# Kernel optimization log

Measured on AMD Instinct MI355X. Metric: run time of the kernel, lower is better.

Reference implementation:

```python
import jax, jax.numpy as jnp
import numpy as np

B, C, W, H = 4, 256, 64, 64
K = C // 8      # key_channels = in_channels // 8
O = C           # out_channels = in_channels


def setup_inputs() -> dict:
    key = jax.random.key(0)
    ks = jax.random.split(key, 8)
    x = jax.random.normal(ks[0], (B, C, W, H), dtype=jnp.float32)
    # 1x1 conv weights stored as [out, in]; conv-style fan-in init scale
    s = 1.0 / np.sqrt(C)
    Wq = jax.random.uniform(ks[1], (K, C), minval=-s, maxval=s, dtype=jnp.float32)
    bq = jax.random.uniform(ks[2], (K,), minval=-s, maxval=s, dtype=jnp.float32)
    Wk = jax.random.uniform(ks[3], (K, C), minval=-s, maxval=s, dtype=jnp.float32)
    bk = jax.random.uniform(ks[4], (K,), minval=-s, maxval=s, dtype=jnp.float32)
    Wv = jax.random.uniform(ks[5], (O, C), minval=-s, maxval=s, dtype=jnp.float32)
    bv = jax.random.uniform(ks[6], (O,), minval=-s, maxval=s, dtype=jnp.float32)
    # gamma is zero-init in the module; use a small nonzero value so the
    # attention branch contributes measurably (kernel-testing baseline)
    gamma = 0.1 * jax.random.normal(ks[7], (1,), dtype=jnp.float32)
    return {"x": x, "Wq": Wq, "bq": bq, "Wk": Wk, "bk": bk,
            "Wv": Wv, "bv": bv, "gamma": gamma}


def reference(x, Wq, bq, Wk, bk, Wv, bv, gamma):
    b, c, w, h = x.shape
    n = w * h
    xr = x.reshape(b, c, n)                                   # B,C,N
    # 1x1 convs == per-pixel linear projections
    q = jnp.einsum('kc,bcn->bnk', Wq, xr) + bq                # B,N,K (permuted query)
    k = jnp.einsum('kc,bcn->bkn', Wk, xr) + bk[:, None]       # B,K,N
    energy = jnp.einsum('bnk,bkm->bnm', q, k)                 # B,N,N
    attention = jax.nn.softmax(energy, axis=-1)
    v = jnp.einsum('oc,bcn->bon', Wv, xr) + bv[:, None]       # B,O,N
    # out = bmm(V, attention^T): out[b,o,m] = sum_n V[b,o,n] * attn[b,m,n]
    out = jnp.einsum('bon,bmn->bom', v, attention)
    out = out.reshape(b, O, w, h)
    out = gamma * out + x                                     # true skip connection
    return out, attention
```

## Files before the change

### kernel.cpp

```cpp
#include <hip/hip_runtime.h>

#define NB  4
#define CCH 256
#define NN  4096
#define KD  32
#define OD  256

typedef __attribute__((ext_vector_type(8))) __bf16 bf16x8;
typedef __attribute__((ext_vector_type(4))) float  floatx4;

__device__ __forceinline__ unsigned short f2bf(float f) {
    union { float f; unsigned u; } v; v.f = f;
    unsigned r = v.u + 0x7FFFu + ((v.u >> 16) & 1u);
    return (unsigned short)(r >> 16);
}
__device__ __forceinline__ float bf2f(unsigned short h) {
    union { unsigned u; float f; } v; v.u = ((unsigned)h) << 16;
    return v.f;
}
__device__ __forceinline__ bf16x8 ldfrag(const unsigned short* p) {
    union { bf16x8 v; unsigned u[4]; } r;
    r.u[0] = *(const unsigned*)(p + 0);
    r.u[1] = *(const unsigned*)(p + 2);
    r.u[2] = *(const unsigned*)(p + 4);
    r.u[3] = *(const unsigned*)(p + 6);
    return r.v;
}

#define WPAD 66
#define VPAD 136

__global__ __launch_bounds__(256) void proj_kernel(
    const float* __restrict__ x,
    const float* __restrict__ Wq, const float* __restrict__ bq,
    const float* __restrict__ Wk, const float* __restrict__ bk,
    const float* __restrict__ Wv, const float* __restrict__ bv,
    unsigned short* __restrict__ Qb, unsigned short* __restrict__ Ktb,
    unsigned short* __restrict__ Vb)
{
    __shared__ __align__(16) unsigned char smem[50944];
    unsigned short* Wh   = (unsigned short*)smem;
    unsigned short* Wl   = (unsigned short*)(smem + 8448);
    unsigned short* Xth  = (unsigned short*)(smem + 16896);
    unsigned short* Xtl  = (unsigned short*)(smem + 33792);
    float*          bias = (float*)(smem + 50688);
    unsigned short* Yt = (unsigned short*)(smem + 16896);
    unsigned short* Vt = (unsigned short*)(smem + 16896);

    const int bid = blockIdx.x;
    const int mc  = bid >> 7;
    const int pnl = bid & 127;
    const int nb  = pnl & 31;
    const int b   = pnl >> 5;

    const int tid = threadIdx.x;
    const int wave = tid >> 6;
    const int lane = tid & 63;
    const int quad = lane >> 4;
    const int li   = lane & 15;
    const int pxw  = wave * 32;
    const int px0  = nb * 128;

    const float* xb = x + (size_t)b * CCH * NN;

    floatx4 acc[4][2];
    #pragma unroll
    for (int mf = 0; mf < 4; ++mf)
        #pragma unroll
        for (int nf = 0; nf < 2; ++nf)
            acc[mf][nf] = (floatx4){0.f, 0.f, 0.f, 0.f};

    for (int ks = 0; ks < 4; ++ks) {
        const int c0 = ks * 64;
        __syncthreads();

        #pragma unroll
        for (int i = 0; i < 4; ++i) {
            int idx4 = i * 256 + tid;
            int row  = idx4 >> 4;
            int c4   = (idx4 & 15) * 4;
            const float* src;
            if (mc == 0) src = (row < 32) ? (Wq + row * CCH) : (Wk + (row - 32) * CCH);
            else         src = Wv + ((size_t)((mc - 1) * 64 + row)) * CCH;
            floatx4 w = *(const floatx4*)(src + c0 + c4);
            #pragma unroll
            for (int j = 0; j < 4; ++j) {
                unsigned short h = f2bf(w[j]);
                unsigned short l = f2bf(w[j] - bf2f(h));
                Wh[row * WPAD + c4 + j] = h;
                Wl[row * WPAD + c4 + j] = l;
            }
        }
        #pragma unroll
        for (int i = 0; i < 8; ++i) {
            int idx4 = i * 256 + tid;
            int c    = idx4 >> 5;
            int px   = (idx4 & 31) * 4;
            floatx4 v = *(const floatx4*)(xb + (size_t)(c0 + c) * NN + px0 + px);
            #pragma unroll
            for (int j = 0; j < 4; ++j) {
                unsigned short h = f2bf(v[j]);
                unsigned short l = f2bf(v[j] - bf2f(h));
                Xth[(px + j) * WPAD + c] = h;
                Xtl[(px + j) * WPAD + c] = l;
            }
        }
        if (ks == 0 && tid < 64) {
            float bb;
            if (mc == 0) bb = (tid < 32) ? bq[tid] : bk[tid - 32];
            else         bb = bv[(mc - 1) * 64 + tid];
            bias[tid] = bb;
        }
        __syncthreads();

        #pragma unroll
        for (int kk = 0; kk < 2; ++kk) {
            bf16x8 ah[4], al[4], bh[2], bl[2];
            #pragma unroll
            for (int mf = 0; mf < 4; ++mf) {
                const int ro = (mf * 16 + li) * WPAD + kk * 32 + quad * 8;
                ah[mf] = ldfrag(Wh + ro);
                al[mf] = ldfrag(Wl + ro);
            }
            #pragma unroll
            for (int nf = 0; nf < 2; ++nf) {
                const int ro = (pxw + nf * 16 + li) * WPAD + kk * 32 + quad * 8;
                bh[nf] = ldfrag(Xth + ro);
                bl[nf] = ldfrag(Xtl + ro);
            }
            #pragma unroll
            for (int mf = 0; mf < 4; ++mf)
                #pragma unroll
                for (int nf = 0; nf < 2; ++nf) {
                    acc[mf][nf] = __builtin_amdgcn_mfma_f32_16x16x32_bf16(ah[mf], bh[nf], acc[mf][nf], 0, 0, 0);
                    acc[mf][nf] = __builtin_amdgcn_mfma_f32_16x16x32_bf16(ah[mf], bl[nf], acc[mf][nf], 0, 0, 0);
                    acc[mf][nf] = __builtin_amdgcn_mfma_f32_16x16x32_bf16(al[mf], bh[nf], acc[mf][nf], 0, 0, 0);
                }
        }
    }

    __syncthreads();
    if (mc == 0) {
        #pragma unroll
        for (int mf = 0; mf < 4; ++mf)
            #pragma unroll
            for (int nf = 0; nf < 2; ++nf)
                #pragma unroll
                for (int r = 0; r < 4; ++r) {
                    const int o = mf * 16 + quad * 4 + r;
                    float f = acc[mf][nf][r] + bias[o];
                    Yt[(pxw + nf * 16 + li) * WPAD + o] = f2bf(f);
                }
        __syncthreads();
        if (tid < 128) {
            const int px = tid;
            const size_t n = (size_t)(b * NN + px0 + px);
            unsigned short* qdst = Qb  + n * KD;
            unsigned short* kdst = Ktb + n * KD;
            const unsigned short* src = Yt + px * WPAD;
            #pragma unroll
            for (int i = 0; i < 4; ++i) {
                union { uint4 u4; unsigned u[4]; } q, k;
                #pragma unroll
                for (int j = 0; j < 4; ++j) {
                    q.u[j] = *(const unsigned*)(src + i * 8 + j * 2);
                    k.u[j] = *(const unsigned*)(src + 32 + i * 8 + j * 2);
                }
                *(uint4*)(qdst + i * 8) = q.u4;
                *(uint4*)(kdst + i * 8) = k.u4;
            }
        }
    } else {
        #pragma unroll
        for (int mf = 0; mf < 4; ++mf)
            #pragma unroll
            for (int nf = 0; nf < 2; ++nf)
                #pragma unroll
                for (int r = 0; r < 4; ++r) {
                    const int o = mf * 16 + quad * 4 + r;
                    float f = acc[mf][nf][r] + bias[o];
                    Vt[o * VPAD + pxw + nf * 16 + li] = f2bf(f);
                }
        __syncthreads();
        const int ol   = tid >> 2;
        const int part = tid & 3;
        const unsigned short* src = Vt + ol * VPAD + part * 32;
        unsigned short* dst = Vb + (size_t)(b * OD + (mc - 1) * 64 + ol) * NN + px0 + part * 32;
        *(uint4*)(dst + 0) = *(const uint4*)(src + 0);
        *(uint4*)(dst + 8) = *(const uint4*)(src + 8);
        *(uint4*)(dst + 16) = *(const uint4*)(src + 16);
        *(uint4*)(dst + 24) = *(const uint4*)(src + 24);
    }
}

__global__ __launch_bounds__(512, 2) void attn_kernel(
    const float* __restrict__ x, const float* __restrict__ gammap,
    const unsigned short* __restrict__ Qb,
    const unsigned short* __restrict__ Ktb,
    const unsigned short* __restrict__ Vb,
    float* __restrict__ out, float* __restrict__ attn)
{
    __shared__ __align__(16) unsigned char smem[59904];
    unsigned short* Vlds  = (unsigned short*)smem;
    float*          panel = (float*)(smem + 40960);
    float*          sred  = (float*)(smem + 59392);

    const int tid  = threadIdx.x;
    const int wave = tid >> 6;
    const int lane = tid & 63;
    const int quad = lane >> 4;
    const int li   = lane & 15;
    const int g    = wave & 3;
    const int h    = wave >> 2;

    const int bid = blockIdx.x;
    const int b   = (bid & 7) >> 1;
    const int mt  = ((bid >> 3) << 1) | (bid & 1);
    const int mw  = mt * 64;
    const int hb  = h * 2048;

    unsigned short* Vh  = Vlds + h * 10240;
    float*          pan = panel + wave * 576;

    const floatx4 zero = {0.f, 0.f, 0.f, 0.f};

    const bf16x8 aQ = *(const bf16x8*)(Qb + (size_t)(b * NN + mw + g * 16 + li) * KD + quad * 8);
    const unsigned short* ktbase = Ktb + (size_t)b * NN * KD + quad * 8;

    float lrow[4] = {0.f, 0.f, 0.f, 0.f};
    #pragma unroll 4
    for (int nt = 0; nt < 128; ++nt) {
        bf16x8 bK = *(const bf16x8*)(ktbase + (size_t)(hb + nt * 16 + li) * KD);
        floatx4 s = __builtin_amdgcn_mfma_f32_16x16x32_bf16(aQ, bK, zero, 0, 0, 0);
        #pragma unroll
        for (int r = 0; r < 4; ++r) lrow[r] += __expf(s[r]);
    }
    #pragma unroll
    for (int r = 0; r < 4; ++r) {
        #pragma unroll
        for (int xm = 1; xm < 16; xm <<= 1)
            lrow[r] += __shfl_xor(lrow[r], xm);
    }
    if (li == 0) {
        #pragma unroll
        for (int r = 0; r < 4; ++r) sred[(g * 2 + h) * 16 + quad * 4 + r] = lrow[r];
    }
    __syncthreads();
    float linv[4];
    #pragma unroll
    for (int r = 0; r < 4; ++r) {
        const int row = quad * 4 + r;
        linv[r] = 1.0f / (sred[(g * 2 + 0) * 16 + row] + sred[(g * 2 + 1) * 16 + row]);
    }

    floatx4 oacc[16];
    #pragma unroll
    for (int ot = 0; ot < 16; ++ot) oacc[ot] = zero;

    const int hs = tid >> 8;
    const int st = tid & 255;
    const unsigned short* vsrc = Vb + (size_t)b * OD * NN + hs * 2048;
    unsigned short*       vdst = Vlds + hs * 10240;

    bf16x8 vtmp[4];
    #pragma unroll
    for (int i = 0; i < 4; ++i) {
        int linear = i * 256 + st;
        int o = linear >> 2, p = linear & 3;
        vtmp[i] = *(const bf16x8*)(vsrc + (size_t)o * NN + p * 8);
    }
    bf16x8 bK0 = *(const bf16x8*)(ktbase + (size_t)(hb + li) * KD);
    bf16x8 bK1 = *(const bf16x8*)(ktbase + (size_t)(hb + 16 + li) * KD);

    for (int c = 0; c < 64; ++c) {
        __builtin_amdgcn_s_barrier();

        #pragma unroll
        for (int i = 0; i < 4; ++i) {
            int linear = i * 256 + st;
            int o = linear >> 2, p = linear & 3;
            *(bf16x8*)(vdst + o * 40 + p * 8) = vtmp[i];
        }
        asm volatile("s_waitcnt lgkmcnt(0)" ::: "memory");
        __builtin_amdgcn_s_barrier();

        floatx4 s0 = __builtin_amdgcn_mfma_f32_16x16x32_bf16(aQ, bK0, zero, 0, 0, 0);
        floatx4 s1 = __builtin_amdgcn_mfma_f32_16x16x32_bf16(aQ, bK1, zero, 0, 0, 0);

        bf16x8 nK0, nK1;
        if (c < 63) {
            const int n1 = hb + (c + 1) * 32;
            nK0 = *(const bf16x8*)(ktbase + (size_t)(n1 + li) * KD);
            nK1 = *(const bf16x8*)(ktbase + (size_t)(n1 + 16 + li) * KD);
            #pragma unroll
            for (int i = 0; i < 4; ++i) {
                int linear = i * 256 + st;
                int o = linear >> 2, p = linear & 3;
                vtmp[i] = *(const bf16x8*)(vsrc + (size_t)o * NN + (c + 1) * 32 + p * 8);
            }
        }

        #pragma unroll
        for (int r = 0; r < 4; ++r) {
            float p0 = __expf(s0[r]) * linv[r];
            float p1 = __expf(s1[r]) * linv[r];
            const int row = quad * 4 + r;
            pan[row * 36 + li]      = p0;
            pan[row * 36 + 16 + li] = p1;
        }
        {
            const float* prow = pan + li * 36 + quad * 8;
            floatx4 pa = *(const floatx4*)(prow);
            floatx4 pb = *(const floatx4*)(prow + 4);
            union { bf16x8 v; unsigned short s[8]; } ap;
            #pragma unroll
            for (int j = 0; j < 4; ++j) {
                ap.s[j]     = f2bf(pa[j]);
                ap.s[4 + j] = f2bf(pb[j]);
            }
            #pragma unroll
            for (int ot = 0; ot < 16; ++ot) {
                bf16x8 bV = *(const bf16x8*)(Vh + (ot * 16 + li) * 40 + quad * 8);
                oacc[ot] = __builtin_amdgcn_mfma_f32_16x16x32_bf16(ap.v, bV, oacc[ot], 0, 0, 0);
            }
        }
        {
            float* ab = attn + ((size_t)(b * NN + mw + g * 16)) * NN + hb + c * 32;
            #pragma unroll
            for (int it = 0; it < 2; ++it) {
                int row = it * 8 + (lane >> 3);
                int c4  = (lane & 7) * 4;
                floatx4 v = *(const floatx4*)(pan + row * 36 + c4);
                *(floatx4*)(ab + (size_t)row * NN + c4) = v;
            }
        }
        bK0 = bK1;
        if (c < 63) { bK0 = nK0; bK1 = nK1; }
    }

    const float gm = gammap[0];
    float* Olds = (float*)(void*)smem;
    #pragma unroll 1
    for (int p = 0; p < 2; ++p) {
        __syncthreads();
        if (h == 0 && (g >> 1) == p) {
            #pragma unroll
            for (int ot = 0; ot < 16; ++ot)
                #pragma unroll
                for (int r = 0; r < 4; ++r)
                    Olds[(ot * 16 + li) * 36 + (g & 1) * 16 + quad * 4 + r] = oacc[ot][r];
        }
        __syncthreads();
        if (h == 1 && (g >> 1) == p) {
            #pragma unroll
            for (int ot = 0; ot < 16; ++ot)
                #pragma unroll
                for (int r = 0; r < 4; ++r)
                    Olds[(ot * 16 + li) * 36 + (g & 1) * 16 + quad * 4 + r] += oacc[ot][r];
        }
        __syncthreads();
        #pragma unroll
        for (int it = 0; it < 4; ++it) {
            int linear = it * 512 + tid;
            int o = linear >> 3, seg = linear & 7;
            floatx4 ov = *(const floatx4*)(Olds + o * 36 + seg * 4);
            size_t gidx = (size_t)(b * OD + o) * NN + mw + p * 32 + seg * 4;
            floatx4 xv = *(const floatx4*)(x + gidx);
            floatx4 res;
            res[0] = gm * ov[0] + xv[0];
            res[1] = gm * ov[1] + xv[1];
            res[2] = gm * ov[2] + xv[2];
            res[3] = gm * ov[3] + xv[3];
            *(floatx4*)(out + gidx) = res;
        }
    }
}

extern "C" void kernel_launch(void* const* d_in, const int* in_sizes, int n_in,
                              void* d_out, int out_size, void* d_ws, size_t ws_size,
                              hipStream_t stream) {
    const float* x     = (const float*)d_in[0];
    const float* Wq    = (const float*)d_in[1];
    const float* bq    = (const float*)d_in[2];
    const float* Wk    = (const float*)d_in[3];
    const float* bk    = (const float*)d_in[4];
    const float* Wv    = (const float*)d_in[5];
    const float* bv    = (const float*)d_in[6];
    const float* gamma = (const float*)d_in[7];

    float* out  = (float*)d_out;
    float* attn = out + (size_t)NB * OD * NN;

    unsigned short* Qb  = (unsigned short*)d_ws;
    unsigned short* Ktb = Qb  + (size_t)NB * NN * KD;
    unsigned short* Vb  = Ktb + (size_t)NB * NN * KD;

    proj_kernel<<<dim3(640), 256, 0, stream>>>(x, Wq, bq, Wk, bk, Wv, bv, Qb, Ktb, Vb);
    attn_kernel<<<dim3(256), 512, 0, stream>>>(x, gamma, Qb, Ktb, Vb, out, attn);
}
```

Before: 435.8 us.

## Split attention matrix write into separate kernel and defer softmax normalization

The fused attention kernel no longer runs a separate row-sum pass before the PV loop. It accumulates the softmax denominator during the main loop and rescales the output at the end, then stores the inverse row sums to workspace. A new kernel recomputes QK^T with 1024 blocks, normalizes the scores and streams the 256MB attention matrix with wider coalesced row stores. This takes the large attention store out of the MFMA-bound PV loop and spreads it over more blocks, at the cost of computing QK^T and exp a second time.

```diff
diff --git a/kernel.cpp b/kernel.cpp
--- a/kernel.cpp
+++ b/kernel.cpp
@@ -193,17 +193,18 @@
     }
 }
 
-__global__ __launch_bounds__(512, 2) void attn_kernel(
+__global__ __launch_bounds__(512, 2) void attn_pv_kernel(
     const float* __restrict__ x, const float* __restrict__ gammap,
     const unsigned short* __restrict__ Qb,
     const unsigned short* __restrict__ Ktb,
     const unsigned short* __restrict__ Vb,
-    float* __restrict__ out, float* __restrict__ attn)
+    float* __restrict__ out, float* __restrict__ linvG)
 {
-    __shared__ __align__(16) unsigned char smem[59904];
+    __shared__ __align__(16) unsigned char smem[60160];
     unsigned short* Vlds  = (unsigned short*)smem;
     float*          panel = (float*)(smem + 40960);
-    float*          sred  = (float*)(smem + 59392);
+    float*          sredL = (float*)(smem + 59392);
+    float*          lf    = (float*)(smem + 59904);
 
     const int tid  = threadIdx.x;
     const int wave = tid >> 6;
@@ -227,35 +228,10 @@
     const bf16x8 aQ = *(const bf16x8*)(Qb + (size_t)(b * NN + mw + g * 16 + li) * KD + quad * 8);
     const unsigned short* ktbase = Ktb + (size_t)b * NN * KD + quad * 8;
 
-    float lrow[4] = {0.f, 0.f, 0.f, 0.f};
-    #pragma unroll 4
-    for (int nt = 0; nt < 128; ++nt) {
-        bf16x8 bK = *(const bf16x8*)(ktbase + (size_t)(hb + nt * 16 + li) * KD);
-        floatx4 s = __builtin_amdgcn_mfma_f32_16x16x32_bf16(aQ, bK, zero, 0, 0, 0);
-        #pragma unroll
-        for (int r = 0; r < 4; ++r) lrow[r] += __expf(s[r]);
-    }
-    #pragma unroll
-    for (int r = 0; r < 4; ++r) {
-        #pragma unroll
-        for (int xm = 1; xm < 16; xm <<= 1)
-            lrow[r] += __shfl_xor(lrow[r], xm);
-    }
-    if (li == 0) {
-        #pragma unroll
-        for (int r = 0; r < 4; ++r) sred[(g * 2 + h) * 16 + quad * 4 + r] = lrow[r];
-    }
-    __syncthreads();
-    float linv[4];
-    #pragma unroll
-    for (int r = 0; r < 4; ++r) {
-        const int row = quad * 4 + r;
-        linv[r] = 1.0f / (sred[(g * 2 + 0) * 16 + row] + sred[(g * 2 + 1) * 16 + row]);
-    }
-
     floatx4 oacc[16];
     #pragma unroll
     for (int ot = 0; ot < 16; ++ot) oacc[ot] = zero;
+    float lrow[4] = {0.f, 0.f, 0.f, 0.f};
 
     const int hs = tid >> 8;
     const int st = tid & 255;
@@ -274,7 +250,6 @@
 
     for (int c = 0; c < 64; ++c) {
         __builtin_amdgcn_s_barrier();
-
         #pragma unroll
         for (int i = 0; i < 4; ++i) {
             int linear = i * 256 + st;
@@ -302,8 +277,10 @@
 
         #pragma unroll
         for (int r = 0; r < 4; ++r) {
-            float p0 = __expf(s0[r]) * linv[r];
-            float p1 = __expf(s1[r]) * linv[r];
+            float p0 = __expf(s0[r]);
+            float p1 = __expf(s1[r]);
+            lrow[r] += p0;
+            lrow[r] += p1;
             const int row = quad * 4 + r;
             pan[row * 36 + li]      = p0;
             pan[row * 36 + 16 + li] = p1;
@@ -324,19 +301,28 @@
                 oacc[ot] = __builtin_amdgcn_mfma_f32_16x16x32_bf16(ap.v, bV, oacc[ot], 0, 0, 0);
             }
         }
-        {
-            float* ab = attn + ((size_t)(b * NN + mw + g * 16)) * NN + hb + c * 32;
-            #pragma unroll
-            for (int it = 0; it < 2; ++it) {
-                int row = it * 8 + (lane >> 3);
-                int c4  = (lane & 7) * 4;
-                floatx4 v = *(const floatx4*)(pan + row * 36 + c4);
-                *(floatx4*)(ab + (size_t)row * NN + c4) = v;
-            }
-        }
         bK0 = bK1;
         if (c < 63) { bK0 = nK0; bK1 = nK1; }
     }
+
+    #pragma unroll
+    for (int r = 0; r < 4; ++r) {
+        #pragma unroll
+        for (int xm = 1; xm < 16; xm <<= 1)
+            lrow[r] += __shfl_xor(lrow[r], xm);
+    }
+    if (li == 0) {
+        #pragma unroll
+        for (int r = 0; r < 4; ++r)
+            sredL[h * 64 + g * 16 + quad * 4 + r] = lrow[r];
+    }
+    __syncthreads();
+    if (tid < 64) {
+        float inv = 1.0f / (sredL[tid] + sredL[64 + tid]);
+        lf[tid] = inv;
+        linvG[b * NN + mw + tid] = inv;
+    }
+    __syncthreads();
 
     const float gm = gammap[0];
     float* Olds = (float*)(void*)smem;
@@ -364,14 +350,81 @@
             int linear = it * 512 + tid;
             int o = linear >> 3, seg = linear & 7;
             floatx4 ov = *(const floatx4*)(Olds + o * 36 + seg * 4);
+            floatx4 lv = *(const floatx4*)(lf + p * 32 + seg * 4);
             size_t gidx = (size_t)(b * OD + o) * NN + mw + p * 32 + seg * 4;
             floatx4 xv = *(const floatx4*)(x + gidx);
             floatx4 res;
-            res[0] = gm * ov[0] + xv[0];
-            res[1] = gm * ov[1] + xv[1];
-            res[2] = gm * ov[2] + xv[2];
-            res[3] = gm * ov[3] + xv[3];
+            res[0] = gm * ov[0] * lv[0] + xv[0];
+            res[1] = gm * ov[1] * lv[1] + xv[1];
+            res[2] = gm * ov[2] * lv[2] + xv[2];
+            res[3] = gm * ov[3] * lv[3] + xv[3];
             *(floatx4*)(out + gidx) = res;
+        }
+    }
+}
+
+__global__ __launch_bounds__(256, 2) void attn_write_kernel(
+    const unsigned short* __restrict__ Qb,
+    const unsigned short* __restrict__ Ktb,
+    const float* __restrict__ linvG,
+    float* __restrict__ attn)
+{
+    __shared__ __align__(16) float pan[4][16 * 264];
+
+    const int tid  = threadIdx.x;
+    const int w    = tid >> 6;
+    const int lane = tid & 63;
+    const int quad = lane >> 4;
+    const int li   = lane & 15;
+
+    const int bid = blockIdx.x;
+    const int b   = (bid & 7) >> 1;
+    const int mt  = ((bid >> 3) << 1) | (bid & 1);
+    const int mw  = mt * 16;
+    const int nq  = w * 1024;
+
+    const floatx4 zero = {0.f, 0.f, 0.f, 0.f};
+    float* mypan = pan[w];
+
+    const bf16x8 aQ = *(const bf16x8*)(Qb + (size_t)(b * NN + mw + li) * KD + quad * 8);
+    const unsigned short* ktbase = Ktb + (size_t)b * NN * KD + quad * 8;
+
+    float linv_[4];
+    #pragma unroll
+    for (int r = 0; r < 4; ++r)
+        linv_[r] = linvG[b * NN + mw + quad * 4 + r];
+
+    bf16x8 bK0 = *(const bf16x8*)(ktbase + (size_t)(nq + li) * KD);
+    bf16x8 bK1 = *(const bf16x8*)(ktbase + (size_t)(nq + 16 + li) * KD);
+
+    for (int c = 0; c < 32; ++c) {
+        const int cc = c & 7;
+        floatx4 s0 = __builtin_amdgcn_mfma_f32_16x16x32_bf16(aQ, bK0, zero, 0, 0, 0);
+        floatx4 s1 = __builtin_amdgcn_mfma_f32_16x16x32_bf16(aQ, bK1, zero, 0, 0, 0);
+
+        if (c < 31) {
+            const int n1 = nq + (c + 1) * 32;
+            bK0 = *(const bf16x8*)(ktbase + (size_t)(n1 + li) * KD);
+            bK1 = *(const bf16x8*)(ktbase + (size_t)(n1 + 16 + li) * KD);
+        }
+
+        #pragma unroll
+        for (int r = 0; r < 4; ++r) {
+            float p0 = __expf(s0[r]) * linv_[r];
+            float p1 = __expf(s1[r]) * linv_[r];
+            const int row = quad * 4 + r;
+            mypan[row * 264 + cc * 32 + li]      = p0;
+            mypan[row * 264 + cc * 32 + 16 + li] = p1;
+        }
+
+        if (cc == 7) {
+            const int f = c >> 3;
+            float* ab = attn + ((size_t)(b * NN + mw)) * NN + nq + f * 256 + lane * 4;
+            #pragma unroll
+            for (int j = 0; j < 16; ++j) {
+                floatx4 v = *(const floatx4*)(mypan + j * 264 + lane * 4);
+                *(floatx4*)(ab + (size_t)j * NN) = v;
+            }
         }
     }
 }
@@ -394,7 +447,9 @@
     unsigned short* Qb  = (unsigned short*)d_ws;
     unsigned short* Ktb = Qb  + (size_t)NB * NN * KD;
     unsigned short* Vb  = Ktb + (size_t)NB * NN * KD;
+    float*          linvG = (float*)(Vb + (size_t)NB * OD * NN);
 
     proj_kernel<<<dim3(640), 256, 0, stream>>>(x, Wq, bq, Wk, bk, Wv, bv, Qb, Ktb, Vb);
-    attn_kernel<<<dim3(256), 512, 0, stream>>>(x, gamma, Qb, Ktb, Vb, out, attn);
-}
+    attn_pv_kernel<<<dim3(256), 512, 0, stream>>>(x, gamma, Qb, Ktb, Vb, out, linvG);
+    attn_write_kernel<<<dim3(1024), 256, 0, stream>>>(Qb, Ktb, linvG, attn);
+}
```

After: 454.0 us. +4.2%, slower.
